# Kernel optimization log

Measured on AMD Instinct MI355X. Metric: run time of the kernel, lower is better.

Reference implementation:

```python
import math
import jax, jax.numpy as jnp
import numpy as np

IN_CH = 256
BIG, SMALL = 15, 3
GHOST_RATIO = 0.23
NK = math.ceil(BIG / SMALL)           # 5
PAD = SMALL // 2                       # 1
MID = BIG // 2                         # 7
REAL_PAD = [MID - i * SMALL - PAD for i in range(NK)]  # [6,3,0,-3,-6]

# Replicate the torch module's deterministic ghost/rep channel split
np.random.seed(123)
_ghostN = int(IN_CH * GHOST_RATIO)     # 58
REPN = IN_CH - _ghostN                 # 198
_ghost = np.sort(np.random.choice(IN_CH, _ghostN, replace=False))
_rep = np.array(sorted(set(range(IN_CH)) - set(_ghost.tolist())), dtype=np.int64)

B, L = 32, 4096
EPS = 1e-5


def _bn(x, g, b):
    # training-mode BatchNorm1d over (B, L) per channel
    m = jnp.mean(x, (0, 2), keepdims=True)
    v = jnp.var(x, (0, 2), keepdims=True)
    return (x - m) * jax.lax.rsqrt(v + EPS) * g[None, :, None] + b[None, :, None]


def _shift(x, p):
    # zero-filled shift along L: out[t] = x[t - p]
    Lx = x.shape[-1]
    if p > 0:
        return jnp.pad(x, ((0, 0), (0, 0), (p, 0)))[..., :Lx]
    if p < 0:
        return jnp.pad(x, ((0, 0), (0, 0), (0, -p)))[..., -Lx:]
    return x


def setup_inputs() -> dict:
    key = jax.random.key(0)
    ks = jax.random.split(key, 3)
    inputs = jax.random.normal(ks[0], (B, IN_CH, L), dtype=jnp.float32)
    lora_w1 = jax.random.normal(ks[1], (REPN * NK, 1, SMALL), dtype=jnp.float32) * 0.1
    lora_w2 = jax.random.normal(ks[2], (REPN * NK, 1, SMALL), dtype=jnp.float32) * 0.1
    ones = jnp.ones((REPN,), jnp.float32)
    zeros = jnp.zeros((REPN,), jnp.float32)
    return {"inputs": inputs, "lora_w1": lora_w1, "lora_w2": lora_w2,
            "gamma1": ones, "beta1": zeros, "gamma2": ones, "beta2": zeros,
            "gamma3": ones, "beta3": zeros}


def reference(inputs, lora_w1, lora_w2, gamma1, beta1, gamma2, beta2, gamma3, beta3):
    rep_in = inputs[:, _rep, :]        # [B, repN, L]
    ghost_in = inputs[:, _ghost, :]    # [B, ghostN, L]
    # sum of N_path depthwise convs == one conv with summed weights
    w = lora_w1 + lora_w2              # [repN*nk, 1, small]
    out = jax.lax.conv_general_dilated(
        rep_in, w, window_strides=(1,), padding=[(PAD, PAD)],
        dimension_numbers=("NCH", "OIH", "NCH"), feature_group_count=REPN)
    b, _, l = out.shape
    o = out.reshape(b, REPN, NK, l)    # torch grouped conv: group-major channel order
    # shift-add decomposition: reconstruct big-kernel responses from nk small-conv slices
    x1 = sum(_shift(o[:, :, i, :], REAL_PAD[i]) for i in range(NK))
    x2 = sum(_shift(o[:, :, i, :], -REAL_PAD[i]) for i in range(NK))
    x3 = o[:, :, NK // 2, :]           # zero-shift (small-kernel) slice
    x1 = _bn(x1, gamma1, beta1)
    x2 = _bn(x2, gamma2, beta2)
    x3 = _bn(x3, gamma3, beta3)
    x = x1 + x2 + x3 + rep_in
    return jnp.concatenate([x, ghost_in], axis=1)  # [B, C, L]
```

## Files before the change

### kernel.cpp

```cpp
#include <hip/hip_runtime.h>

#define LEN 4096
#define BATCH 32
#define CH 256
#define REPN 198
#define GHOSTN 58
#define NROW (REPN * BATCH)
#define NGHOST (GHOSTN * BATCH)
#define P1REPBLK 1584

typedef float f32x4 __attribute__((ext_vector_type(4)));

struct MTState { unsigned mt[624]; int mti; };
struct Tab { int rep[REPN]; int ghost[GHOSTN]; };

static constexpr unsigned mt_next(MTState& s) {
    if (s.mti >= 624) {
        for (int k = 0; k < 624; ++k) {
            unsigned y = (s.mt[k] & 0x80000000u) | (s.mt[(k + 1) % 624] & 0x7fffffffu);
            s.mt[k] = s.mt[(k + 397) % 624] ^ (y >> 1) ^ ((y & 1u) ? 0x9908b0dfu : 0u);
        }
        s.mti = 0;
    }
    unsigned y = s.mt[s.mti++];
    y ^= y >> 11;
    y ^= (y << 7) & 0x9d2c5680u;
    y ^= (y << 15) & 0xefc60000u;
    y ^= y >> 18;
    return y;
}

static constexpr Tab make_tab() {
    MTState s{};
    s.mt[0] = 123u;
    for (int i = 1; i < 624; ++i)
        s.mt[i] = 1812433253u * (s.mt[i - 1] ^ (s.mt[i - 1] >> 30)) + (unsigned)i;
    s.mti = 624;
    int perm[256] = {};
    for (int i = 0; i < 256; ++i) perm[i] = i;
    for (int i = 255; i > 0; --i) {
        unsigned mask = (unsigned)i;
        mask |= mask >> 1; mask |= mask >> 2; mask |= mask >> 4;
        mask |= mask >> 8; mask |= mask >> 16;
        unsigned j = 0;
        do { j = mt_next(s) & mask; } while (j > (unsigned)i);
        int t = perm[i]; perm[i] = perm[j]; perm[j] = t;
    }
    bool g[256] = {};
    for (int k = 0; k < GHOSTN; ++k) g[perm[k]] = true;
    Tab t{};
    int rc = 0, gc = 0;
    for (int c = 0; c < 256; ++c) {
        if (g[c]) t.ghost[gc++] = c;
        else      t.rep[rc++] = c;
    }
    return t;
}

__constant__ Tab d_tab = make_tab();

#define C1F(D) wb[(D) / 3][(D) % 3]
#define C2F(D) wb[4 - (D) / 3][(D) % 3]

__global__ __launch_bounds__(256) void pass1_kernel(const float* __restrict__ x,
                                                    const float* __restrict__ w1,
                                                    const float* __restrict__ w2,
                                                    float* __restrict__ stats_ws,
                                                    float* __restrict__ out) {
    const int blk = blockIdx.x;
    if (blk >= P1REPBLK) {
        const int g = (blk - P1REPBLK) % GHOSTN;
        const int b = (blk - P1REPBLK) / GHOSTN;
        const int ch = d_tab.ghost[g];
        const f32x4* src = (const f32x4*)(x + ((size_t)b * CH + ch) * LEN);
        f32x4* dst = (f32x4*)(out + ((size_t)b * CH + REPN + g) * LEN);
#pragma unroll
        for (int k = 0; k < 4; ++k) {
            f32x4 t = __builtin_nontemporal_load(&src[threadIdx.x + 256 * k]);
            dst[threadIdx.x + 256 * k] = t;
        }
        return;
    }

    const int wv = (blk << 2) | (threadIdx.x >> 6);
    const int lane = threadIdx.x & 63;
    const int r = wv % REPN;
    const int b = wv / REPN;
    const float* row = x + ((size_t)b * CH + d_tab.rep[r]) * LEN;

    float A[15];
#pragma unroll
    for (int dl = 0; dl < 15; ++dl) A[dl] = 0.f;
    float SX = 0.f;
    float B0[8], B1[8], B2[8], B3[8], B4[8];
    const int base = lane << 6;

#define LOAD8(DST, OFF)                                                           \
    {                                                                             \
        if ((OFF) < LEN) {                                                        \
            const f32x4* q4_ = (const f32x4*)(row + (OFF));                       \
            f32x4 u0_ = q4_[0], u1_ = q4_[1];                                     \
            DST[0] = u0_.x; DST[1] = u0_.y; DST[2] = u0_.z; DST[3] = u0_.w;       \
            DST[4] = u1_.x; DST[5] = u1_.y; DST[6] = u1_.z; DST[7] = u1_.w;       \
        } else {                                                                  \
            _Pragma("unroll")                                                     \
            for (int t = 0; t < 8; ++t) DST[t] = 0.f;                             \
        }                                                                         \
    }

#define ACC8(P, Q, R)                                                             \
    {                                                                             \
        _Pragma("unroll")                                                         \
        for (int j = 0; j < 8; ++j) {                                             \
            const float xj_ = P[j];                                               \
            SX += xj_;                                                            \
            _Pragma("unroll")                                                     \
            for (int dl = 0; dl < 15; ++dl) {                                     \
                const int t_ = j + dl;                                            \
                const float xd_ = (t_ < 8) ? P[t_]                                \
                                 : (t_ < 16) ? Q[t_ - 8] : R[t_ - 16];            \
                A[dl] = fmaf(xj_, xd_, A[dl]);                                    \
            }                                                                     \
        }                                                                         \
    }

    LOAD8(B0, base);
    LOAD8(B1, base + 8);
    LOAD8(B2, base + 16);
    LOAD8(B3, base + 24);
    LOAD8(B4, base + 32);
    ACC8(B0, B1, B2);  LOAD8(B0, base + 40);
    ACC8(B1, B2, B3);  LOAD8(B1, base + 48);
    ACC8(B2, B3, B4);  LOAD8(B2, base + 56);
    ACC8(B3, B4, B0);  LOAD8(B3, base + 64);
    ACC8(B4, B0, B1);  LOAD8(B4, base + 72);
    ACC8(B0, B1, B2);
    ACC8(B1, B2, B3);
    ACC8(B2, B3, B4);
#undef LOAD8
#undef ACC8

    float wb[5][3];
    {
        const float* p1 = w1 + r * 15;
        const float* p2 = w2 + r * 15;
#pragma unroll
        for (int i = 0; i < 5; ++i)
#pragma unroll
            for (int t = 0; t < 3; ++t) wb[i][t] = p1[i * 3 + t] + p2[i * 3 + t];
    }

    float d1 = 0.f, d1q = 0.f, d2 = 0.f, d2q = 0.f, d3 = 0.f, d3q = 0.f;
    if (lane < 26) {
        const int l = (lane <= 12) ? (lane - 7) : (4090 + (lane - 13));
        float u1 = 0.f, u2 = 0.f, u3 = 0.f, g1 = 0.f, g2 = 0.f;
#pragma unroll
        for (int d = 0; d < 15; ++d) {
            const int p = l + d - 7;
            const float xd = ((unsigned)p < (unsigned)LEN) ? row[p] : 0.f;
            const float a1 = C1F(d) * xd;
            const float a2 = C2F(d) * xd;
            u1 += a1; u2 += a2;
            if (d >= 6 && d <= 8) u3 += a1;
            const bool gate = ((unsigned)(l - 6 + 3 * (d / 3)) < (unsigned)LEN);
            g1 += gate ? a1 : 0.f;
            g2 += gate ? a2 : 0.f;
        }
        if ((unsigned)l < (unsigned)LEN) {
            d1 = g1 - u1;  d1q = fmaf(g1, g1, -u1 * u1);
            d2 = g2 - u2;  d2q = fmaf(g2, g2, -u2 * u2);
        } else {
            d1 = -u1;  d1q = -u1 * u1;
            d2 = -u2;  d2q = -u2 * u2;
            d3 = -u3;  d3q = -u3 * u3;
        }
    }

#pragma unroll
    for (int off = 32; off > 0; off >>= 1) {
#pragma unroll
        for (int dl = 0; dl < 15; ++dl) A[dl] += __shfl_down(A[dl], off);
        SX += __shfl_down(SX, off);
        d1 += __shfl_down(d1, off);   d1q += __shfl_down(d1q, off);
        d2 += __shfl_down(d2, off);   d2q += __shfl_down(d2q, off);
        d3 += __shfl_down(d3, off);   d3q += __shfl_down(d3q, off);
    }

    if (lane == 0) {
        float sq1 = 0.f, sq2 = 0.f;
#pragma unroll
        for (int dl = 0; dl < 15; ++dl) {
            float r1 = 0.f, r2 = 0.f;
#pragma unroll
            for (int d = 0; d + dl < 15; ++d) {
                r1 = fmaf(C1F(d), C1F(d + dl), r1);
                r2 = fmaf(C2F(d), C2F(d + dl), r2);
            }
            const float wA = (dl ? 2.f : 1.f) * A[dl];
            sq1 = fmaf(r1, wA, sq1);
            sq2 = fmaf(r2, wA, sq2);
        }
        const float c30 = wb[2][0], c31 = wb[2][1], c32 = wb[2][2];
        float sq3 = (c30 * c30 + c31 * c31 + c32 * c32) * A[0]
                  + 2.f * (c30 * c31 + c31 * c32) * A[1]
                  + 2.f * (c30 * c32) * A[2];
        float cs = 0.f;
#pragma unroll
        for (int i = 0; i < 5; ++i)
#pragma unroll
            for (int t = 0; t < 3; ++t) cs += wb[i][t];
        const float c3s = c30 + c31 + c32;

        stats_ws[(0 * REPN + r) * BATCH + b] = fmaf(cs, SX, d1);
        stats_ws[(1 * REPN + r) * BATCH + b] = sq1 + d1q;
        stats_ws[(2 * REPN + r) * BATCH + b] = fmaf(cs, SX, d2);
        stats_ws[(3 * REPN + r) * BATCH + b] = sq2 + d2q;
        stats_ws[(4 * REPN + r) * BATCH + b] = fmaf(c3s, SX, d3);
        stats_ws[(5 * REPN + r) * BATCH + b] = sq3 + d3q;
    }
}

__device__ __forceinline__ void load_fast(const float* __restrict__ row, int e, float* v) {
    const f32x4* q4 = (const f32x4*)(row + e - 8);
#pragma unroll
    for (int t = 0; t < 5; ++t) {
        f32x4 u = q4[t];
        v[4 * t] = u.x; v[4 * t + 1] = u.y; v[4 * t + 2] = u.z; v[4 * t + 3] = u.w;
    }
}

__device__ __forceinline__ void load_slow(const float* __restrict__ row, int e, float* v) {
#pragma unroll
    for (int d = 0; d < 20; ++d) {
        int fi = e - 8 + d;
        v[d] = ((unsigned)fi < (unsigned)LEN) ? row[fi] : 0.f;
    }
}

__global__ __launch_bounds__(256) void pass2_kernel(const float* __restrict__ x,
                                                    const float* __restrict__ w1,
                                                    const float* __restrict__ w2,
                                                    const float* __restrict__ stats_ws,
                                                    const float* __restrict__ g1, const float* __restrict__ b1,
                                                    const float* __restrict__ g2, const float* __restrict__ b2,
                                                    const float* __restrict__ g3, const float* __restrict__ b3,
                                                    float* __restrict__ out) {
    const int wv = (blockIdx.x << 2) | (threadIdx.x >> 6);
    const int lane = threadIdx.x & 63;
    const int r = wv % REPN;
    const int b = wv / REPN;
    const int ch = d_tab.rep[r];
    const float* row = x + ((size_t)b * CH + ch) * LEN;

    float p[6];
    const int bb = lane & 31;
#pragma unroll
    for (int q = 0; q < 6; ++q) p[q] = stats_ws[(q * REPN + r) * BATCH + bb];
#pragma unroll
    for (int m = 1; m < 32; m <<= 1)
#pragma unroll
        for (int q = 0; q < 6; ++q) p[q] += __shfl_xor(p[q], m);

    const double invN = 1.0 / (double)(BATCH * LEN);
    float sc[3], sh[3];
    {
        const float gr[3] = {g1[r], g2[r], g3[r]};
        const float br[3] = {b1[r], b2[r], b3[r]};
#pragma unroll
        for (int q = 0; q < 3; ++q) {
            double mean = (double)p[2 * q] * invN;
            double var = (double)p[2 * q + 1] * invN - mean * mean;
            double inv = 1.0 / sqrt(var + 1e-5);
            double scale = (double)gr[q] * inv;
            sc[q] = (float)scale;
            sh[q] = (float)((double)br[q] - mean * scale);
        }
    }
    const float base = sh[0] + sh[1] + sh[2];

    float wb[5][3];
    const float* p1 = w1 + r * 15;
    const float* p2 = w2 + r * 15;
#pragma unroll
    for (int i = 0; i < 5; ++i)
#pragma unroll
        for (int t = 0; t < 3; ++t) wb[i][t] = p1[i * 3 + t] + p2[i * 3 + t];

    float c[15];
#pragma unroll
    for (int k = 0; k < 5; ++k)
#pragma unroll
        for (int t = 0; t < 3; ++t)
            c[3 * k + t] = fmaf(sc[0], wb[k][t], sc[1] * wb[4 - k][t]);
#pragma unroll
    for (int t = 0; t < 3; ++t) c[6 + t] = fmaf(sc[2], wb[2][t], c[6 + t]);

    float* orow = out + ((size_t)b * CH + r) * LEN;
    float vA[20], vB[20];

#define INTERIOR_QUAD(E, V)                                                       \
    {                                                                             \
        float o[4];                                                               \
        _Pragma("unroll")                                                         \
        for (int j = 0; j < 4; ++j) {                                             \
            float acc = base + V[j + 8];                                          \
            _Pragma("unroll")                                                     \
            for (int d = 0; d < 15; ++d) acc = fmaf(c[d], V[j + 1 + d], acc);     \
            o[j] = acc;                                                           \
        }                                                                         \
        f32x4 t = {o[0], o[1], o[2], o[3]};                                       \
        *(f32x4*)(orow + (E)) = t;                                                \
    }

#define EDGE_QUAD(E, V)                                                           \
    {                                                                             \
        float o[4];                                                               \
        _Pragma("unroll")                                                         \
        for (int j = 0; j < 4; ++j) {                                             \
            const int l = (E) + j;                                                \
            float x1 = 0.f, x2 = 0.f, x3 = 0.f;                                   \
            _Pragma("unroll")                                                     \
            for (int i = 0; i < 5; ++i) {                                         \
                float a1 = fmaf(wb[i][0], V[j + 1 + 3 * i],                       \
                           fmaf(wb[i][1], V[j + 2 + 3 * i],                       \
                                wb[i][2] * V[j + 3 + 3 * i]));                    \
                float a2 = fmaf(wb[i][0], V[j + 13 - 3 * i],                      \
                           fmaf(wb[i][1], V[j + 14 - 3 * i],                      \
                                wb[i][2] * V[j + 15 - 3 * i]));                   \
                if (i == 2) x3 = a1;                                              \
                a1 = ((unsigned)(l - 6 + 3 * i) < (unsigned)LEN) ? a1 : 0.f;      \
                a2 = ((unsigned)(l + 6 - 3 * i) < (unsigned)LEN) ? a2 : 0.f;      \
                x1 += a1; x2 += a2;                                               \
            }                                                                     \
            o[j] = fmaf(sc[0], x1, fmaf(sc[1], x2, fmaf(sc[2], x3, base + V[j + 8]))); \
        }                                                                         \
        f32x4 t = {o[0], o[1], o[2], o[3]};                                       \
        *(f32x4*)(orow + (E)) = t;                                                \
    }

    {
        const int e = 4 * lane;
        if (lane < 2) { load_slow(row, e, vA); EDGE_QUAD(e, vA); }
        else          { load_fast(row, e, vA); INTERIOR_QUAD(e, vA); }
    }
    load_fast(row, 4 * lane + 256, vA);
#pragma unroll
    for (int kk = 0; kk < 7; ++kk) {
        const int k = 1 + 2 * kk;
        const int eA = 4 * lane + 256 * k;
        const int eB = eA + 256;
        load_fast(row, eB, vB);
        INTERIOR_QUAD(eA, vA);
        if (kk < 6) load_fast(row, eB + 256, vA);
        INTERIOR_QUAD(eB, vB);
    }
    {
        const int e = 4 * lane + 3840;
        if (lane >= 62) { load_slow(row, e, vA); EDGE_QUAD(e, vA); }
        else            { load_fast(row, e, vA); INTERIOR_QUAD(e, vA); }
    }
#undef INTERIOR_QUAD
#undef EDGE_QUAD
}

extern "C" void kernel_launch(void* const* d_in, const int* in_sizes, int n_in,
                              void* d_out, int out_size, void* d_ws, size_t ws_size,
                              hipStream_t stream) {
    const float* x  = (const float*)d_in[0];
    const float* w1 = (const float*)d_in[1];
    const float* w2 = (const float*)d_in[2];
    const float* g1 = (const float*)d_in[3];
    const float* b1 = (const float*)d_in[4];
    const float* g2 = (const float*)d_in[5];
    const float* b2 = (const float*)d_in[6];
    const float* g3 = (const float*)d_in[7];
    const float* b3 = (const float*)d_in[8];
    float* out = (float*)d_out;
    float* stats_ws = (float*)d_ws;

    pass1_kernel<<<P1REPBLK + NGHOST, 256, 0, stream>>>(x, w1, w2, stats_ws, out);
    pass2_kernel<<<1584, 256, 0, stream>>>(x, w1, w2, stats_ws,
                                           g1, b1, g2, b2, g3, b3, out);
}
```

Measured before the change: 84.01 us.

## Split each row across two wavefronts in both passes and combine stats via LDS

Each (batch, channel) row is now processed by two wavefronts instead of one, doubling the block count in both the statistics pass and the output pass. In pass 1 each half computes partial autocorrelation sums over 2048 elements, and the partials are combined through shared memory after a block barrier. In pass 2 each wave handles half of the row, with edge handling only at the row ends. The aim is more parallelism and shorter per-wave serial work, so memory latency is hidden better. The cost is extra waves, a __syncthreads, and doubled per-wave setup such as loading weights and reducing the BN stats.

Result: faster. 78.53 us (-6.5%).

```diff
diff --git a/kernel.cpp b/kernel.cpp
--- a/kernel.cpp
+++ b/kernel.cpp
@@ -7,7 +7,8 @@
 #define GHOSTN 58
 #define NROW (REPN * BATCH)
 #define NGHOST (GHOSTN * BATCH)
-#define P1REPBLK 1584
+#define P1REPBLK 3168
+#define P2REPBLK 3168
 
 typedef float f32x4 __attribute__((ext_vector_type(4)));
 
@@ -82,18 +83,21 @@
         return;
     }
 
-    const int wv = (blk << 2) | (threadIdx.x >> 6);
+    __shared__ float comb[4][22];
+    const int widx = threadIdx.x >> 6;
     const int lane = threadIdx.x & 63;
-    const int r = wv % REPN;
-    const int b = wv / REPN;
+    const int rowid = (blk << 1) | (widx >> 1);
+    const int half = widx & 1;
+    const int r = rowid % REPN;
+    const int b = rowid / REPN;
     const float* row = x + ((size_t)b * CH + d_tab.rep[r]) * LEN;
 
     float A[15];
 #pragma unroll
     for (int dl = 0; dl < 15; ++dl) A[dl] = 0.f;
     float SX = 0.f;
-    float B0[8], B1[8], B2[8], B3[8], B4[8];
-    const int base = lane << 6;
+    float B0[8], B1[8], B2[8], B3[8], B4[8], B5[8];
+    const int base = (half << 11) + (lane << 5);
 
 #define LOAD8(DST, OFF)                                                           \
     {                                                                             \
@@ -129,14 +133,11 @@
     LOAD8(B2, base + 16);
     LOAD8(B3, base + 24);
     LOAD8(B4, base + 32);
-    ACC8(B0, B1, B2);  LOAD8(B0, base + 40);
-    ACC8(B1, B2, B3);  LOAD8(B1, base + 48);
-    ACC8(B2, B3, B4);  LOAD8(B2, base + 56);
-    ACC8(B3, B4, B0);  LOAD8(B3, base + 64);
-    ACC8(B4, B0, B1);  LOAD8(B4, base + 72);
+    LOAD8(B5, base + 40);
     ACC8(B0, B1, B2);
     ACC8(B1, B2, B3);
     ACC8(B2, B3, B4);
+    ACC8(B3, B4, B5);
 #undef LOAD8
 #undef ACC8
 
@@ -151,7 +152,7 @@
     }
 
     float d1 = 0.f, d1q = 0.f, d2 = 0.f, d2q = 0.f, d3 = 0.f, d3q = 0.f;
-    if (lane < 26) {
+    if (half == 0 && lane < 26) {
         const int l = (lane <= 12) ? (lane - 7) : (4090 + (lane - 13));
         float u1 = 0.f, u2 = 0.f, u3 = 0.f, g1 = 0.f, g2 = 0.f;
 #pragma unroll
@@ -187,6 +188,27 @@
     }
 
     if (lane == 0) {
+#pragma unroll
+        for (int dl = 0; dl < 15; ++dl) comb[widx][dl] = A[dl];
+        comb[widx][15] = SX;
+        comb[widx][16] = d1;  comb[widx][17] = d1q;
+        comb[widx][18] = d2;  comb[widx][19] = d2q;
+        comb[widx][20] = d3;  comb[widx][21] = d3q;
+    }
+    __syncthreads();
+
+    if (half == 0 && lane == 0) {
+        float Af[15];
+#pragma unroll
+        for (int dl = 0; dl < 15; ++dl) Af[dl] = comb[widx][dl] + comb[widx + 1][dl];
+        const float SXf = comb[widx][15] + comb[widx + 1][15];
+        const float e1  = comb[widx][16] + comb[widx + 1][16];
+        const float e1q = comb[widx][17] + comb[widx + 1][17];
+        const float e2  = comb[widx][18] + comb[widx + 1][18];
+        const float e2q = comb[widx][19] + comb[widx + 1][19];
+        const float e3  = comb[widx][20] + comb[widx + 1][20];
+        const float e3q = comb[widx][21] + comb[widx + 1][21];
+
         float sq1 = 0.f, sq2 = 0.f;
 #pragma unroll
         for (int dl = 0; dl < 15; ++dl) {
@@ -196,14 +218,14 @@
                 r1 = fmaf(C1F(d), C1F(d + dl), r1);
                 r2 = fmaf(C2F(d), C2F(d + dl), r2);
             }
-            const float wA = (dl ? 2.f : 1.f) * A[dl];
+            const float wA = (dl ? 2.f : 1.f) * Af[dl];
             sq1 = fmaf(r1, wA, sq1);
             sq2 = fmaf(r2, wA, sq2);
         }
         const float c30 = wb[2][0], c31 = wb[2][1], c32 = wb[2][2];
-        float sq3 = (c30 * c30 + c31 * c31 + c32 * c32) * A[0]
-                  + 2.f * (c30 * c31 + c31 * c32) * A[1]
-                  + 2.f * (c30 * c32) * A[2];
+        float sq3 = (c30 * c30 + c31 * c31 + c32 * c32) * Af[0]
+                  + 2.f * (c30 * c31 + c31 * c32) * Af[1]
+                  + 2.f * (c30 * c32) * Af[2];
         float cs = 0.f;
 #pragma unroll
         for (int i = 0; i < 5; ++i)
@@ -211,12 +233,12 @@
             for (int t = 0; t < 3; ++t) cs += wb[i][t];
         const float c3s = c30 + c31 + c32;
 
-        stats_ws[(0 * REPN + r) * BATCH + b] = fmaf(cs, SX, d1);
-        stats_ws[(1 * REPN + r) * BATCH + b] = sq1 + d1q;
-        stats_ws[(2 * REPN + r) * BATCH + b] = fmaf(cs, SX, d2);
-        stats_ws[(3 * REPN + r) * BATCH + b] = sq2 + d2q;
-        stats_ws[(4 * REPN + r) * BATCH + b] = fmaf(c3s, SX, d3);
-        stats_ws[(5 * REPN + r) * BATCH + b] = sq3 + d3q;
+        stats_ws[(0 * REPN + r) * BATCH + b] = fmaf(cs, SXf, e1);
+        stats_ws[(1 * REPN + r) * BATCH + b] = sq1 + e1q;
+        stats_ws[(2 * REPN + r) * BATCH + b] = fmaf(cs, SXf, e2);
+        stats_ws[(3 * REPN + r) * BATCH + b] = sq2 + e2q;
+        stats_ws[(4 * REPN + r) * BATCH + b] = fmaf(c3s, SXf, e3);
+        stats_ws[(5 * REPN + r) * BATCH + b] = sq3 + e3q;
     }
 }
 
@@ -247,8 +269,10 @@
                                                     float* __restrict__ out) {
     const int wv = (blockIdx.x << 2) | (threadIdx.x >> 6);
     const int lane = threadIdx.x & 63;
-    const int r = wv % REPN;
-    const int b = wv / REPN;
+    const int rowid = wv >> 1;
+    const int half = wv & 1;
+    const int r = rowid % REPN;
+    const int b = rowid / REPN;
     const int ch = d_tab.rep[r];
     const float* row = x + ((size_t)b * CH + ch) * LEN;
 
@@ -338,26 +362,42 @@
         *(f32x4*)(orow + (E)) = t;                                                \
     }
 
-    {
-        const int e = 4 * lane;
-        if (lane < 2) { load_slow(row, e, vA); EDGE_QUAD(e, vA); }
-        else          { load_fast(row, e, vA); INTERIOR_QUAD(e, vA); }
-    }
-    load_fast(row, 4 * lane + 256, vA);
-#pragma unroll
-    for (int kk = 0; kk < 7; ++kk) {
-        const int k = 1 + 2 * kk;
-        const int eA = 4 * lane + 256 * k;
-        const int eB = eA + 256;
-        load_fast(row, eB, vB);
-        INTERIOR_QUAD(eA, vA);
-        if (kk < 6) load_fast(row, eB + 256, vA);
-        INTERIOR_QUAD(eB, vB);
-    }
-    {
-        const int e = 4 * lane + 3840;
-        if (lane >= 62) { load_slow(row, e, vA); EDGE_QUAD(e, vA); }
-        else            { load_fast(row, e, vA); INTERIOR_QUAD(e, vA); }
+    if (half == 0) {
+        {
+            const int e = 4 * lane;
+            if (lane < 2) { load_slow(row, e, vA); EDGE_QUAD(e, vA); }
+            else          { load_fast(row, e, vA); INTERIOR_QUAD(e, vA); }
+        }
+        load_fast(row, 4 * lane + 256, vA);
+#pragma unroll
+        for (int kk = 0; kk < 3; ++kk) {
+            const int k = 1 + 2 * kk;
+            const int eA = 4 * lane + 256 * k;
+            const int eB = eA + 256;
+            load_fast(row, eB, vB);
+            INTERIOR_QUAD(eA, vA);
+            load_fast(row, eB + 256, vA);
+            INTERIOR_QUAD(eB, vB);
+        }
+        INTERIOR_QUAD(4 * lane + 256 * 7, vA);
+    } else {
+        load_fast(row, 4 * lane + 256 * 8, vA);
+#pragma unroll
+        for (int kk = 0; kk < 3; ++kk) {
+            const int k = 8 + 2 * kk;
+            const int eA = 4 * lane + 256 * k;
+            const int eB = eA + 256;
+            load_fast(row, eB, vB);
+            INTERIOR_QUAD(eA, vA);
+            load_fast(row, eB + 256, vA);
+            INTERIOR_QUAD(eB, vB);
+        }
+        INTERIOR_QUAD(4 * lane + 256 * 14, vA);
+        {
+            const int e = 4 * lane + 3840;
+            if (lane >= 62) { load_slow(row, e, vA); EDGE_QUAD(e, vA); }
+            else            { load_fast(row, e, vA); INTERIOR_QUAD(e, vA); }
+        }
     }
 #undef INTERIOR_QUAD
 #undef EDGE_QUAD
@@ -379,6 +419,6 @@
     float* stats_ws = (float*)d_ws;
 
     pass1_kernel<<<P1REPBLK + NGHOST, 256, 0, stream>>>(x, w1, w2, stats_ws, out);
-    pass2_kernel<<<1584, 256, 0, stream>>>(x, w1, w2, stats_ws,
-                                           g1, b1, g2, b2, g3, b3, out);
-}
+    pass2_kernel<<<P2REPBLK, 256, 0, stream>>>(x, w1, w2, stats_ws,
+                                               g1, b1, g2, b2, g3, b3, out);
+}
```
